# Kernel optimization log

Measured on AMD Instinct MI355X. Metric: run time of the kernel, lower is better.

The kernel has to match this reference:

```python
import jax, jax.numpy as jnp
import numpy as np

B, N, A, D = 16, 256, 64, 256


def setup_inputs() -> dict:
    key = jax.random.key(0)
    ks = jax.random.split(key, 9)
    s = 1.0 / np.sqrt(D)
    return {
        "cc_embeds": jax.random.normal(ks[0], (B, N, D), jnp.float32),
        "anchor_embeds": jax.random.normal(ks[1], (B, N, A, D), jnp.float32),
        "sims": jax.random.normal(ks[2], (B, N, A), jnp.float32),
        "Wq": jax.random.normal(ks[3], (D, D), jnp.float32) * s,
        "bq": jax.random.normal(ks[4], (D,), jnp.float32) * s,
        "Wk": jax.random.normal(ks[5], (D, D), jnp.float32) * s,
        "bk": jax.random.normal(ks[6], (D,), jnp.float32) * s,
        "Wv": jax.random.normal(ks[7], (D, D), jnp.float32) * s,
        "bv": jax.random.normal(ks[8], (D,), jnp.float32) * s,
    }


def reference(cc_embeds, anchor_embeds, sims, Wq, bq, Wk, bk, Wv, bv):
    # Linear projections (torch nn.Linear: x @ W.T + b)
    Q = cc_embeds @ Wq.T + bq                    # [B, N, D]
    K = anchor_embeds @ Wk.T + bk                # [B, N, A, D]
    V = anchor_embeds @ Wv.T + bv                # [B, N, A, D]
    scale = 1.0 / jnp.sqrt(jnp.asarray(D, Q.dtype))
    scores = jnp.einsum('bnd,bnad->bna', Q, K) * scale  # [B, N, A]
    adj = scores + sims                          # additive similarity bias
    # conditional softmax: rows whose raw sum == 0 are passed through unchanged
    nonzero = jnp.sum(adj, axis=-1, keepdims=True) != 0
    probs = jnp.where(nonzero, jax.nn.softmax(adj, axis=-1), adj)
    out = jnp.einsum('bna,bnad->bnd', probs, V)  # [B, N, D]
    return out[:, :, None, :]                    # match torch output [B, N, 1, D]
```

## Files before the change

kernel.cpp:

```cpp
#include <hip/hip_runtime.h>
#include <hip/hip_bf16.h>


typedef float f4 __attribute__((ext_vector_type(4)));

__device__ __forceinline__ float bcast_lane(float x, int lane) {
  return __int_as_float(__builtin_amdgcn_readlane(__float_as_int(x), lane));
}

__global__ __launch_bounds__(256) void k1_prep(
    const float* __restrict__ Wq, const float* __restrict__ bq,
    const float* __restrict__ Wk, const float* __restrict__ bk,
    const float* __restrict__ Wv,
    float* __restrict__ M, float* __restrict__ rvec, float* __restrict__ uvec,
    float* __restrict__ s0, float* __restrict__ WvT) {
  __shared__ float colL[256];
  __shared__ float pr[256];
  __shared__ float tile[64][65];
  const int tid = threadIdx.x;
  const int bid = blockIdx.x;
  if (bid < 256) {
    colL[tid] = Wq[tid * 256 + bid];
    __syncthreads();
    float acc = 0.f;
#pragma unroll 4
    for (int d = 0; d < 256; ++d) acc += colL[d] * Wk[d * 256 + tid];
    M[bid * 256 + tid] = acc;
  } else if (bid == 256) {
    colL[tid] = bq[tid];
    __syncthreads();
    float acc = 0.f;
#pragma unroll 4
    for (int d = 0; d < 256; ++d) acc += colL[d] * Wk[d * 256 + tid];
    rvec[tid] = acc;
  } else if (bid == 257) {
    colL[tid] = bk[tid];
    pr[tid] = bq[tid] * bk[tid];
    __syncthreads();
    float acc = 0.f;
#pragma unroll 4
    for (int d = 0; d < 256; ++d) acc += Wq[d * 256 + tid] * colL[d];
    uvec[tid] = acc;
    if (tid == 0) {
      float s = 0.f;
      for (int d = 0; d < 256; ++d) s += pr[d];
      s0[0] = s;
    }
  } else {
    const int tb = bid - 258, bi = tb >> 2, bj = tb & 3;
#pragma unroll
    for (int k = 0; k < 16; ++k) {
      int idx = k * 256 + tid;
      int r = idx >> 6, cL = idx & 63;
      tile[r][cL] = Wv[(bi * 64 + r) * 256 + bj * 64 + cL];
    }
    __syncthreads();
#pragma unroll
    for (int k = 0; k < 16; ++k) {
      int idx = k * 256 + tid;
      int r = idx >> 6, cL = idx & 63;
      WvT[(bj * 64 + r) * 256 + bi * 64 + cL] = tile[cL][r];
    }
  }
}

__global__ __launch_bounds__(256) void k_main(
    const float* __restrict__ cc, const float* __restrict__ anchor,
    const float* __restrict__ sims,
    const float* __restrict__ M, const float* __restrict__ rvec,
    const float* __restrict__ uvec, const float* __restrict__ s0p,
    const float* __restrict__ WvT, const float* __restrict__ bv,
    float* __restrict__ out) {
  __shared__ __align__(16) float pOut[4][8][256];
  __shared__ __align__(16) float t8[8][256];
  __shared__ __align__(16) float w8[8][256];
  __shared__ float cpart[4][8];
  __shared__ float c8[8];
  __shared__ float ps8[8];
  __shared__ float sL[64];
  __shared__ float pL[64];
  const int tid = threadIdx.x;
  const int w = tid >> 6, L = tid & 63;
  const int i0 = blockIdx.x * 8;
  const int e0 = w * 64;

  float ccreg[8];
#pragma unroll
  for (int r = 0; r < 8; ++r) ccreg[r] = cc[(size_t)(i0 + r) * 256 + e0 + L];
  float uvl = uvec[e0 + L];
  {
    f4 acc[8] = {};
#pragma unroll 8
    for (int ee = 0; ee < 64; ++ee) {
      f4 m = *(const f4*)(M + (size_t)(e0 + ee) * 256 + 4 * L);
#pragma unroll
      for (int r = 0; r < 8; ++r) {
        float cv = bcast_lane(ccreg[r], ee);
        acc[r].x += cv * m.x; acc[r].y += cv * m.y;
        acc[r].z += cv * m.z; acc[r].w += cv * m.w;
      }
    }
#pragma unroll
    for (int r = 0; r < 8; ++r) *(f4*)&pOut[w][r][4 * L] = acc[r];
#pragma unroll
    for (int r = 0; r < 8; ++r) {
      float pc = ccreg[r] * uvl;
#pragma unroll
      for (int off = 32; off >= 1; off >>= 1) pc += __shfl_xor(pc, off, 64);
      if (L == 0) cpart[w][r] = pc;
    }
  }

  const f4* g4 = (const f4*)(anchor + (size_t)i0 * 16384);
  f4 v[16];
#pragma unroll
  for (int k = 0; k < 16; ++k) v[k] = __builtin_nontemporal_load(g4 + k * 256 + tid);

  __syncthreads();
  {
    float rv = rvec[tid];
#pragma unroll
    for (int r = 0; r < 8; ++r)
      t8[r][tid] = pOut[0][r][tid] + pOut[1][r][tid] + pOut[2][r][tid] +
                   pOut[3][r][tid] + rv;
    if (tid < 8)
      c8[tid] = cpart[0][tid] + cpart[1][tid] + cpart[2][tid] + cpart[3][tid] + s0p[0];
  }
  __syncthreads();

  float* pW = &pOut[0][0][0];
  for (int r = 0; r < 8; ++r) {
    const f4 t4 = *(const f4*)&t8[r][4 * L];
#pragma unroll
    for (int k = 0; k < 16; ++k) {
      float s = v[k].x * t4.x + v[k].y * t4.y + v[k].z * t4.z + v[k].w * t4.w;
#pragma unroll
      for (int off = 32; off >= 1; off >>= 1) s += __shfl_xor(s, off, 64);
      if (L == 0) sL[k * 4 + w] = s;
    }
    __syncthreads();
    if (tid < 64) {
      float adj = (sL[tid] + c8[r]) * 0.0625f + sims[(size_t)(i0 + r) * 64 + tid];
      float ssum = adj, smax = adj;
#pragma unroll
      for (int off = 32; off >= 1; off >>= 1) {
        ssum += __shfl_xor(ssum, off, 64);
        smax = fmaxf(smax, __shfl_xor(smax, off, 64));
      }
      float p;
      if (ssum != 0.f) {
        p = expf(adj - smax);
        float z = p;
#pragma unroll
        for (int off = 32; off >= 1; off >>= 1) z += __shfl_xor(z, off, 64);
        p = p / z;
      } else {
        p = adj;
      }
      float ps = p;
#pragma unroll
      for (int off = 32; off >= 1; off >>= 1) ps += __shfl_xor(ps, off, 64);
      pL[tid] = p;
      if (tid == 0) ps8[r] = ps;
    }
    __syncthreads();
    f4 acc = {0.f, 0.f, 0.f, 0.f};
#pragma unroll
    for (int k = 0; k < 16; ++k) {
      float p = pL[k * 4 + w];
      acc.x += p * v[k].x; acc.y += p * v[k].y;
      acc.z += p * v[k].z; acc.w += p * v[k].w;
    }
    if (r < 7) {
      const f4* g4n = (const f4*)(anchor + (size_t)(i0 + r + 1) * 16384);
#pragma unroll
      for (int k = 0; k < 16; ++k)
        v[k] = __builtin_nontemporal_load(g4n + k * 256 + tid);
    }
    *(f4*)&pW[w * 256 + 4 * L] = acc;
    __syncthreads();
    w8[r][tid] = pW[tid] + pW[256 + tid] + pW[512 + tid] + pW[768 + tid];
  }
  __syncthreads();

  {
    float wreg[8];
#pragma unroll
    for (int r = 0; r < 8; ++r) wreg[r] = w8[r][e0 + L];
    f4 acc[8] = {};
#pragma unroll 8
    for (int ee = 0; ee < 64; ++ee) {
      f4 m = *(const f4*)(WvT + (size_t)(e0 + ee) * 256 + 4 * L);
#pragma unroll
      for (int r = 0; r < 8; ++r) {
        float cv = bcast_lane(wreg[r], ee);
        acc[r].x += cv * m.x; acc[r].y += cv * m.y;
        acc[r].z += cv * m.z; acc[r].w += cv * m.w;
      }
    }
#pragma unroll
    for (int r = 0; r < 8; ++r) *(f4*)&pOut[w][r][4 * L] = acc[r];
  }
  __syncthreads();
  {
    float b = bv[tid];
#pragma unroll
    for (int r = 0; r < 8; ++r) {
      float s = pOut[0][r][tid] + pOut[1][r][tid] + pOut[2][r][tid] + pOut[3][r][tid];
      out[(size_t)(i0 + r) * 256 + tid] = s + b * ps8[r];
    }
  }
}

extern "C" void kernel_launch(void* const* d_in, const int* in_sizes, int n_in,
                              void* d_out, int out_size, void* d_ws, size_t ws_size,
                              hipStream_t stream) {
  const float* cc     = (const float*)d_in[0];
  const float* anchor = (const float*)d_in[1];
  const float* sims   = (const float*)d_in[2];
  const float* Wq     = (const float*)d_in[3];
  const float* bq     = (const float*)d_in[4];
  const float* Wk     = (const float*)d_in[5];
  const float* bk     = (const float*)d_in[6];
  const float* Wv     = (const float*)d_in[7];
  const float* bv     = (const float*)d_in[8];
  float* out = (float*)d_out;
  float* ws  = (float*)d_ws;

  float* M    = ws;
  float* WvT  = ws + 65536;
  float* rvec = ws + 131072;
  float* uvec = ws + 131328;
  float* s0   = ws + 131584;

  k1_prep<<<274, 256, 0, stream>>>(Wq, bq, Wk, bk, Wv, M, rvec, uvec, s0, WvT);
  k_main<<<512, 256, 0, stream>>>(cc, anchor, sims, M, rvec, uvec, s0, WvT, bv, out);
}
```

Before: 414.4 us.

## Double-buffer anchor rows and compute softmax redundantly per wave to cut barriers

Result: no change. 412.4 us (-0.5%).

```diff
diff --git a/kernel.cpp b/kernel.cpp
--- a/kernel.cpp
+++ b/kernel.cpp
@@ -1,11 +1,16 @@
 #include <hip/hip_runtime.h>
-#include <hip/hip_bf16.h>
 
 
 typedef float f4 __attribute__((ext_vector_type(4)));
 
 __device__ __forceinline__ float bcast_lane(float x, int lane) {
   return __int_as_float(__builtin_amdgcn_readlane(__float_as_int(x), lane));
+}
+
+__device__ __forceinline__ void sync_lds() {
+  asm volatile("s_waitcnt lgkmcnt(0)" ::: "memory");
+  __builtin_amdgcn_s_barrier();
+  __builtin_amdgcn_sched_barrier(0);
 }
 
 __global__ __launch_bounds__(256) void k1_prep(
@@ -64,7 +69,59 @@
   }
 }
 
-__global__ __launch_bounds__(256) void k_main(
+#define ROW_BODY(R, CUR, PREFETCH_STMT)                                       \
+  {                                                                           \
+    const f4 t4 = *(const f4*)&t8[R][4 * L];                                  \
+    _Pragma("unroll")                                                         \
+    for (int k = 0; k < 16; ++k) {                                            \
+      float s = CUR[k].x * t4.x + CUR[k].y * t4.y + CUR[k].z * t4.z +         \
+                CUR[k].w * t4.w;                                              \
+      _Pragma("unroll")                                                       \
+      for (int off = 32; off >= 1; off >>= 1) s += __shfl_xor(s, off, 64);    \
+      if (L == 0) sL8[R][k * 4 + w] = s;                                      \
+    }                                                                         \
+    sync_lds();                                                               \
+    float adj = (sL8[R][L] + c8[R]) * 0.0625f + simsL[R * 64 + L];            \
+    float ssum = adj, smax = adj;                                             \
+    _Pragma("unroll")                                                         \
+    for (int off = 32; off >= 1; off >>= 1) {                                 \
+      ssum += __shfl_xor(ssum, off, 64);                                      \
+      smax = fmaxf(smax, __shfl_xor(smax, off, 64));                          \
+    }                                                                         \
+    float p;                                                                  \
+    if (ssum != 0.f) {                                                        \
+      p = expf(adj - smax);                                                   \
+      float z = p;                                                            \
+      _Pragma("unroll")                                                       \
+      for (int off = 32; off >= 1; off >>= 1) z += __shfl_xor(z, off, 64);    \
+      p = p / z;                                                              \
+    } else {                                                                  \
+      p = adj;                                          \
+    }                                                                         \
+    float ps = p;                                                             \
+    _Pragma("unroll")                                                         \
+    for (int off = 32; off >= 1; off >>= 1) ps += __shfl_xor(ps, off, 64);    \
+    psr[R] = ps;                                                              \
+    f4 acc = {0.f, 0.f, 0.f, 0.f};                                            \
+    _Pragma("unroll")                                                         \
+    for (int k = 0; k < 16; ++k) {                                            \
+      float pk = bcast_lane(p, k * 4 + w);                                    \
+      acc.x += pk * CUR[k].x; acc.y += pk * CUR[k].y;                         \
+      acc.z += pk * CUR[k].z; acc.w += pk * CUR[k].w;                         \
+    }                                                                         \
+    PREFETCH_STMT;                                                            \
+    *(f4*)&pOut[w][R][4 * L] = acc;                                           \
+  }
+
+#define PF(RN, CUR)                                                           \
+  {                                                                           \
+    const f4* gn = g4 + (size_t)(RN)*4096;                                    \
+    _Pragma("unroll")                                                         \
+    for (int k = 0; k < 16; ++k)                                              \
+      CUR[k] = __builtin_nontemporal_load(gn + k * 256 + tid);                \
+  }
+
+__global__ __launch_bounds__(256, 2) void k_main(
     const float* __restrict__ cc, const float* __restrict__ anchor,
     const float* __restrict__ sims,
     const float* __restrict__ M, const float* __restrict__ rvec,
@@ -73,12 +130,10 @@
     float* __restrict__ out) {
   __shared__ __align__(16) float pOut[4][8][256];
   __shared__ __align__(16) float t8[8][256];
-  __shared__ __align__(16) float w8[8][256];
+  __shared__ float sL8[8][64];
+  __shared__ float simsL[512];
   __shared__ float cpart[4][8];
   __shared__ float c8[8];
-  __shared__ float ps8[8];
-  __shared__ float sL[64];
-  __shared__ float pL[64];
   const int tid = threadIdx.x;
   const int w = tid >> 6, L = tid & 63;
   const int i0 = blockIdx.x * 8;
@@ -88,6 +143,11 @@
 #pragma unroll
   for (int r = 0; r < 8; ++r) ccreg[r] = cc[(size_t)(i0 + r) * 256 + e0 + L];
   float uvl = uvec[e0 + L];
+  float rv_ = rvec[tid];
+  float s0v = s0p[0];
+  simsL[tid] = sims[(size_t)i0 * 64 + tid];
+  simsL[256 + tid] = sims[(size_t)i0 * 64 + 256 + tid];
+
   {
     f4 acc[8] = {};
 #pragma unroll 8
@@ -112,81 +172,39 @@
   }
 
   const f4* g4 = (const f4*)(anchor + (size_t)i0 * 16384);
-  f4 v[16];
-#pragma unroll
-  for (int k = 0; k < 16; ++k) v[k] = __builtin_nontemporal_load(g4 + k * 256 + tid);
-
-  __syncthreads();
+  f4 vA[16], vB[16];
+  PF(0, vA);
+  PF(1, vB);
+
+  sync_lds();
+#pragma unroll
+  for (int r = 0; r < 8; ++r)
+    t8[r][tid] = pOut[0][r][tid] + pOut[1][r][tid] + pOut[2][r][tid] +
+                 pOut[3][r][tid] + rv_;
+  if (tid < 8)
+    c8[tid] = cpart[0][tid] + cpart[1][tid] + cpart[2][tid] + cpart[3][tid] + s0v;
+  sync_lds();
+
+  float psr[8];
+  ROW_BODY(0, vA, PF(2, vA));
+  ROW_BODY(1, vB, PF(3, vB));
+  ROW_BODY(2, vA, PF(4, vA));
+  ROW_BODY(3, vB, PF(5, vB));
+  ROW_BODY(4, vA, PF(6, vA));
+  ROW_BODY(5, vB, PF(7, vB));
+  ROW_BODY(6, vA, );
+  ROW_BODY(7, vB, );
+
+  sync_lds();
+
+  float wreg[8];
+#pragma unroll
+  for (int r = 0; r < 8; ++r)
+    wreg[r] = pOut[0][r][e0 + L] + pOut[1][r][e0 + L] + pOut[2][r][e0 + L] +
+              pOut[3][r][e0 + L];
+  float bvv = bv[tid];
+  sync_lds();
   {
-    float rv = rvec[tid];
-#pragma unroll
-    for (int r = 0; r < 8; ++r)
-      t8[r][tid] = pOut[0][r][tid] + pOut[1][r][tid] + pOut[2][r][tid] +
-                   pOut[3][r][tid] + rv;
-    if (tid < 8)
-      c8[tid] = cpart[0][tid] + cpart[1][tid] + cpart[2][tid] + cpart[3][tid] + s0p[0];
-  }
-  __syncthreads();
-
-  float* pW = &pOut[0][0][0];
-  for (int r = 0; r < 8; ++r) {
-    const f4 t4 = *(const f4*)&t8[r][4 * L];
-#pragma unroll
-    for (int k = 0; k < 16; ++k) {
-      float s = v[k].x * t4.x + v[k].y * t4.y + v[k].z * t4.z + v[k].w * t4.w;
-#pragma unroll
-      for (int off = 32; off >= 1; off >>= 1) s += __shfl_xor(s, off, 64);
-      if (L == 0) sL[k * 4 + w] = s;
-    }
-    __syncthreads();
-    if (tid < 64) {
-      float adj = (sL[tid] + c8[r]) * 0.0625f + sims[(size_t)(i0 + r) * 64 + tid];
-      float ssum = adj, smax = adj;
-#pragma unroll
-      for (int off = 32; off >= 1; off >>= 1) {
-        ssum += __shfl_xor(ssum, off, 64);
-        smax = fmaxf(smax, __shfl_xor(smax, off, 64));
-      }
-      float p;
-      if (ssum != 0.f) {
-        p = expf(adj - smax);
-        float z = p;
-#pragma unroll
-        for (int off = 32; off >= 1; off >>= 1) z += __shfl_xor(z, off, 64);
-        p = p / z;
-      } else {
-        p = adj;
-      }
-      float ps = p;
-#pragma unroll
-      for (int off = 32; off >= 1; off >>= 1) ps += __shfl_xor(ps, off, 64);
-      pL[tid] = p;
-      if (tid == 0) ps8[r] = ps;
-    }
-    __syncthreads();
-    f4 acc = {0.f, 0.f, 0.f, 0.f};
-#pragma unroll
-    for (int k = 0; k < 16; ++k) {
-      float p = pL[k * 4 + w];
-      acc.x += p * v[k].x; acc.y += p * v[k].y;
-      acc.z += p * v[k].z; acc.w += p * v[k].w;
-    }
-    if (r < 7) {
-      const f4* g4n = (const f4*)(anchor + (size_t)(i0 + r + 1) * 16384);
-#pragma unroll
-      for (int k = 0; k < 16; ++k)
-        v[k] = __builtin_nontemporal_load(g4n + k * 256 + tid);
-    }
-    *(f4*)&pW[w * 256 + 4 * L] = acc;
-    __syncthreads();
-    w8[r][tid] = pW[tid] + pW[256 + tid] + pW[512 + tid] + pW[768 + tid];
-  }
-  __syncthreads();
-
-  {
-    float wreg[8];
-#pragma unroll
-    for (int r = 0; r < 8; ++r) wreg[r] = w8[r][e0 + L];
     f4 acc[8] = {};
 #pragma unroll 8
     for (int ee = 0; ee < 64; ++ee) {
@@ -201,14 +219,11 @@
 #pragma unroll
     for (int r = 0; r < 8; ++r) *(f4*)&pOut[w][r][4 * L] = acc[r];
   }
-  __syncthreads();
-  {
-    float b = bv[tid];
-#pragma unroll
-    for (int r = 0; r < 8; ++r) {
-      float s = pOut[0][r][tid] + pOut[1][r][tid] + pOut[2][r][tid] + pOut[3][r][tid];
-      out[(size_t)(i0 + r) * 256 + tid] = s + b * ps8[r];
-    }
+  sync_lds();
+#pragma unroll
+  for (int r = 0; r < 8; ++r) {
+    float s = pOut[0][r][tid] + pOut[1][r][tid] + pOut[2][r][tid] + pOut[3][r][tid];
+    out[(size_t)(i0 + r) * 256 + tid] = s + bvv * psr[r];
   }
 }
 
```
